# Kernel tuning notes

Measured on AMD Instinct MI355X. Metric: run time of the kernel, lower is better.

## Reference

```python
import jax, jax.numpy as jnp
import numpy as np

B, DIN, D, T, C = 32768, 784, 256, 16, 64


def setup_inputs() -> dict:
    key = jax.random.key(0)
    ks = jax.random.split(key, 4)
    x = jax.random.normal(ks[0], (B, DIN), dtype=jnp.float32)
    Wp = jax.random.normal(ks[1], (DIN, D), dtype=jnp.float32) / np.sqrt(DIN).astype(np.float32)
    bp = jnp.zeros((D,), jnp.float32)
    sigs_raw = jax.random.normal(ks[2], (T, D), dtype=jnp.float32) * 0.5
    Wc = jax.random.normal(ks[3], (T, D, C), dtype=jnp.float32) / np.sqrt(D).astype(np.float32)
    bc = jnp.zeros((T, C), jnp.float32)
    return {"x": x, "Wp": Wp, "bp": bp, "sigs_raw": sigs_raw, "Wc": Wc, "bc": bc}


def _quantize_ternary(s):
    # straight-through ternary quantization with +/-0.3 thresholds
    q = jnp.where(s > 0.3, 1.0, jnp.where(s < -0.3, -1.0, 0.0)).astype(s.dtype)
    return s + jax.lax.stop_gradient(q - s)


def reference(x, Wp, bp, sigs_raw, Wc, bc):
    h = x @ Wp + bp                                   # [B, D]
    sigs = _quantize_ternary(sigs_raw)                # [T, D] ternary signatures
    scores = h @ sigs.T                               # [B, T]
    tile_indices = jnp.argmax(scores, axis=-1)        # [B] top-1 routing
    # per-tile linear classifiers, then select the routed tile's logits
    all_logits = jnp.einsum('bd,tdc->btc', h, Wc) + bc[None]   # [B, T, C]
    logits = jnp.take_along_axis(all_logits, tile_indices[:, None, None], axis=1)[:, 0, :]
    return logits, tile_indices
```

## Files before the change

### kernel.cpp

```cpp
#include <hip/hip_runtime.h>

typedef short short8 __attribute__((ext_vector_type(8)));
typedef float f32x4 __attribute__((ext_vector_type(4)));

#define B_ROWS 32768
#define DIN 784
#define D_DIM 256
#define T_TILES 16
#define C_DIM 64
#define BM 64
#define NCHUNK 25

#define WPT_OFF    0u
#define WCT_OFF    409600u
#define WS_OFF     933888u
#define BS_OFF     1036288u
#define H_OFF      1036416u
#define BUCKET_OFF 17813632u
#define CNT_OFF    19910784u

static __device__ inline unsigned short f2bf(float f) {
    unsigned u = __builtin_bit_cast(unsigned, f);
    u += 0x7fffu + ((u >> 16) & 1u);
    return (unsigned short)(u >> 16);
}
static __device__ inline double qtern(float s) {
    double v = (double)s;
    return (v > 0.3) ? 1.0 : ((v < -0.3) ? -1.0 : 0.0);
}

__global__ __launch_bounds__(256)
void prep_kernel(const float* __restrict__ Wp, const float* __restrict__ bp,
                 const float* __restrict__ sigs_raw, const float* __restrict__ Wc,
                 char* __restrict__ ws) {
    __shared__ __align__(16) char u2[34816];
    const int bid = blockIdx.x, tid = threadIdx.x;
    unsigned short* wpt = (unsigned short*)(ws + WPT_OFF);
    unsigned short* wct = (unsigned short*)(ws + WCT_OFF);
    double* Wsd = (double*)(ws + WS_OFF);
    double* bsd = (double*)(ws + BS_OFF);

    if (bid < 25) {
        unsigned short (*lt)[40] = (unsigned short (*)[40])u2;
        const int k0 = bid * 32;
        #pragma unroll
        for (int p = 0; p < 8; ++p) {
            const int k = p * 4 + (tid >> 6);
            const int c = (tid & 63) * 4;
            float4 v = make_float4(0.f, 0.f, 0.f, 0.f);
            if (k0 + k < DIN) v = *(const float4*)&Wp[(size_t)(k0 + k) * D_DIM + c];
            lt[c + 0][k] = f2bf(v.x); lt[c + 1][k] = f2bf(v.y);
            lt[c + 2][k] = f2bf(v.z); lt[c + 3][k] = f2bf(v.w);
        }
        __syncthreads();
        const float4* src = (const float4*)&lt[tid][0];
        float4* dst = (float4*)(wpt + bid * 8192 + tid * 32);
        dst[0] = src[0]; dst[1] = src[1]; dst[2] = src[2]; dst[3] = src[3];
    } else if (bid < 123) {
        float* sigq = (float*)u2;
        float* wp8  = (float*)(u2 + 16384);
        const int k0 = (bid - 25) * 8;
        #pragma unroll
        for (int i = 0; i < 16; ++i) {
            const int idx = i * 256 + tid;
            sigq[idx] = (float)qtern(sigs_raw[idx]);
        }
        #pragma unroll
        for (int i = 0; i < 8; ++i)
            wp8[i * 256 + tid] = Wp[(size_t)(k0 + i) * D_DIM + tid];
        __syncthreads();
        const int kk = tid >> 5, t = (tid >> 1) & 15, half = tid & 1;
        double s = 0.0;
        const float* wr = &wp8[kk * 256 + half * 128];
        const float* sq = &sigq[t * 256 + half * 128];
        for (int d = 0; d < 128; ++d) s += (double)wr[d] * (double)sq[d];
        s += __shfl_xor(s, 1);
        if (half == 0) Wsd[(k0 + kk) * 16 + t] = s;
    } else if (bid < 139) {
        unsigned short (*lc)[264] = (unsigned short (*)[264])u2;
        const int t = bid - 123;
        #pragma unroll
        for (int j = 0; j < 16; ++j) {
            const int f4 = j * 256 + tid;
            const int d  = f4 >> 4;
            const int c4 = (f4 & 15) * 4;
            const float4 v = *(const float4*)&Wc[((size_t)t * D_DIM + d) * C_DIM + c4];
            lc[c4 + 0][d] = f2bf(v.x); lc[c4 + 1][d] = f2bf(v.y);
            lc[c4 + 2][d] = f2bf(v.z); lc[c4 + 3][d] = f2bf(v.w);
        }
        __syncthreads();
        const int c = tid >> 2, d0 = (tid & 3) * 64;
        const float4* src = (const float4*)&lc[c][d0];
        float4* dst = (float4*)(wct + t * 16384 + c * 256 + d0);
        #pragma unroll
        for (int i = 0; i < 8; ++i) dst[i] = src[i];
    } else {
        int* cnt = (int*)(ws + CNT_OFF);
        if (tid < 16) cnt[tid] = 0;
        Wsd[12544 + tid] = 0.0;
        const int t = tid >> 4, l = tid & 15;
        double s = 0.0;
        #pragma unroll
        for (int j = 0; j < 16; ++j) {
            const int d = l * 16 + j;
            s += (double)bp[d] * qtern(sigs_raw[t * D_DIM + d]);
        }
        #pragma unroll
        for (int m = 8; m >= 1; m >>= 1) s += __shfl_xor(s, m);
        if (l == 0) bsd[t] = s;
    }
}

__global__ __launch_bounds__(256, 2)
void gemm_score_kernel(const float* __restrict__ x, const float* __restrict__ bp,
                       char* __restrict__ ws, float* __restrict__ out) {
    __shared__ __align__(16) char u[59904];
    __shared__ int tidx_s[BM];

    unsigned short* Abuf = (unsigned short*)u;
    unsigned short* Bbuf = (unsigned short*)(u + 10240);
    double*         wss  = (double*)(u + 51200);

    const unsigned short* wpt = (const unsigned short*)(ws + WPT_OFF);
    unsigned short* hbf = (unsigned short*)(ws + H_OFF);
    const double* Wsd = (const double*)(ws + WS_OFF);
    const double* bsd = (const double*)(ws + BS_OFF);
    int* bucket = (int*)(ws + BUCKET_OFF);
    int* cnt = (int*)(ws + CNT_OFF);

    const int tid = threadIdx.x;
    const int row0 = blockIdx.x * BM;
    const int wid = tid >> 6, lane = tid & 63;
    const int wr = wid >> 1, wcid = wid & 1;
    const int lrow = lane & 15, kb8 = (lane >> 4) * 8;
    const int ar = tid >> 2, ako = (tid & 3) * 8;
    const int wk = tid >> 3, wt = (tid * 2) & 15;

    f32x4 acc[2][8];
    #pragma unroll
    for (int i = 0; i < 2; ++i)
        #pragma unroll
        for (int j = 0; j < 8; ++j) acc[i][j] = (f32x4){0.f, 0.f, 0.f, 0.f};
    double accd[16];
    #pragma unroll
    for (int t = 0; t < 16; ++t) accd[t] = 0.0;
    float xs8[8];

    {
        const float4* p = (const float4*)&x[(size_t)(row0 + ar) * DIN + ako];
        const float4 a0 = p[0], a1 = p[1];
        xs8[0] = a0.x; xs8[1] = a0.y; xs8[2] = a0.z; xs8[3] = a0.w;
        xs8[4] = a1.x; xs8[5] = a1.y; xs8[6] = a1.z; xs8[7] = a1.w;
        unsigned short tmp[8];
        #pragma unroll
        for (int i = 0; i < 8; ++i) tmp[i] = f2bf(xs8[i]);
        *(short8*)(Abuf + ar * 40 + ako) = *(short8*)tmp;
        const float4* q = (const float4*)(wpt + tid * 32);
        float4* db = (float4*)(Bbuf + tid * 40);
        db[0] = q[0]; db[1] = q[1]; db[2] = q[2]; db[3] = q[3];
        const double w0 = Wsd[tid * 2], w1 = Wsd[tid * 2 + 1];
        wss[wk * 17 + wt] = w0; wss[wk * 17 + wt + 1] = w1;
    }
    __syncthreads();

    for (int c = 0; c < NCHUNK; ++c) {
        const int cur = c & 1;
        const bool more = (c + 1 < NCHUNK);
        float4 va0, va1, vb0, vb1, vb2, vb3;
        double w0 = 0.0, w1 = 0.0;
        if (more) {
            const int kbase = (c + 1) * 32 + ako;
            if (kbase < DIN) {
                const float4* p = (const float4*)&x[(size_t)(row0 + ar) * DIN + kbase];
                va0 = p[0]; va1 = p[1];
            } else {
                va0 = make_float4(0, 0, 0, 0); va1 = make_float4(0, 0, 0, 0);
            }
            const float4* q = (const float4*)(wpt + (c + 1) * 8192 + tid * 32);
            vb0 = q[0]; vb1 = q[1]; vb2 = q[2]; vb3 = q[3];
            w0 = Wsd[(c + 1) * 512 + tid * 2];
            w1 = Wsd[(c + 1) * 512 + tid * 2 + 1];
        }
        {
            const unsigned short* Ab = Abuf + cur * 2560;
            const unsigned short* Bb = Bbuf + cur * 10240;
            const short8 af0 = *(const short8*)(Ab + (wr * 32 + lrow) * 40 + kb8);
            const short8 af1 = *(const short8*)(Ab + (wr * 32 + 16 + lrow) * 40 + kb8);
            #pragma unroll
            for (int cf = 0; cf < 8; ++cf) {
                const short8 bfr = *(const short8*)(Bb + (wcid * 128 + cf * 16 + lrow) * 40 + kb8);
                acc[0][cf] = __builtin_amdgcn_mfma_f32_16x16x32_bf16(af0, bfr, acc[0][cf], 0, 0, 0);
                acc[1][cf] = __builtin_amdgcn_mfma_f32_16x16x32_bf16(af1, bfr, acc[1][cf], 0, 0, 0);
            }
        }
        {
            const double* wbase = wss + cur * 544;
            #pragma unroll
            for (int i = 0; i < 8; ++i) {
                const double xv = (double)xs8[i];
                const double* wrow = wbase + (ako + i) * 17;
                #pragma unroll
                for (int t = 0; t < 16; ++t) accd[t] += xv * wrow[t];
            }
        }
        if (more) {
            xs8[0] = va0.x; xs8[1] = va0.y; xs8[2] = va0.z; xs8[3] = va0.w;
            xs8[4] = va1.x; xs8[5] = va1.y; xs8[6] = va1.z; xs8[7] = va1.w;
            unsigned short tmp[8];
            #pragma unroll
            for (int i = 0; i < 8; ++i) tmp[i] = f2bf(xs8[i]);
            *(short8*)(Abuf + (cur ^ 1) * 2560 + ar * 40 + ako) = *(short8*)tmp;
            float4* db = (float4*)(Bbuf + (cur ^ 1) * 10240 + tid * 40);
            db[0] = vb0; db[1] = vb1; db[2] = vb2; db[3] = vb3;
            wss[(cur ^ 1) * 544 + wk * 17 + wt] = w0;
            wss[(cur ^ 1) * 544 + wk * 17 + wt + 1] = w1;
        }
        __syncthreads();
    }

    unsigned short* h_s = (unsigned short*)u;
    #pragma unroll
    for (int cf = 0; cf < 8; ++cf) {
        const int gc = wcid * 128 + cf * 16 + lrow;
        const float bpv = bp[gc];
        #pragma unroll
        for (int rf = 0; rf < 2; ++rf) {
            const int lr = wr * 32 + rf * 16 + (lane >> 4) * 4;
            #pragma unroll
            for (int r = 0; r < 4; ++r)
                h_s[(lr + r) * 264 + gc] = f2bf(acc[rf][cf][r] + bpv);
        }
    }

    #pragma unroll
    for (int t = 0; t < 16; ++t) {
        accd[t] += __shfl_xor(accd[t], 1);
        accd[t] += __shfl_xor(accd[t], 2);
    }
    if ((tid & 3) == 0) {
        double best = -1.0e300; int bi = 0;
        #pragma unroll
        for (int t = 0; t < 16; ++t) {
            const double v = accd[t] + bsd[t];
            if (v > best) { best = v; bi = t; }
        }
        tidx_s[ar] = bi;
        out[(size_t)B_ROWS * C_DIM + row0 + ar] = (float)bi;
    }
    __syncthreads();

    {
        const int r = tid >> 2, q = tid & 3;
        const float4* src = (const float4*)(h_s + r * 264 + q * 64);
        float4 v[8];
        #pragma unroll
        for (int i = 0; i < 8; ++i) v[i] = src[i];
        float4* dst = (float4*)(hbf + (size_t)(row0 + r) * D_DIM + q * 64);
        #pragma unroll
        for (int i = 0; i < 8; ++i) dst[i] = v[i];
    }

    if (tid < T_TILES) {
        int c = 0;
        for (int r = 0; r < BM; ++r) c += (tidx_s[r] == tid);
        int pos = atomicAdd(&cnt[tid], c);
        for (int r = 0; r < BM; ++r)
            if (tidx_s[r] == tid) bucket[tid * B_ROWS + (pos++)] = row0 + r;
    }
}

__global__ __launch_bounds__(256)
void logits_kernel(const float* __restrict__ bc, const char* __restrict__ ws,
                   float* __restrict__ out) {
    __shared__ __align__(16) unsigned short As[128 * 136];
    __shared__ __align__(16) unsigned short Bs[64 * 136];
    __shared__ int rows_s[128];

    const int tid = threadIdx.x;
    const int t = blockIdx.x >> 8;
    const int c0 = (blockIdx.x & 255) * 128;
    const int* cnt = (const int*)(ws + CNT_OFF);
    const int cntv = cnt[t];
    if (c0 >= cntv) return;

    const int* bucket = (const int*)(ws + BUCKET_OFF);
    const unsigned short* hbf = (const unsigned short*)(ws + H_OFF);
    const unsigned short* wct = (const unsigned short*)(ws + WCT_OFF);

    if (tid < 128) {
        int i = c0 + tid; if (i >= cntv) i = cntv - 1;
        rows_s[tid] = bucket[t * B_ROWS + i];
    }
    __syncthreads();

    const int wid = tid >> 6, lane = tid & 63;
    const int wr = wid >> 1, wcid = wid & 1;
    const int lrow = lane & 15, kb8 = (lane >> 4) * 8;

    f32x4 acc[4][2];
    #pragma unroll
    for (int i = 0; i < 4; ++i) { acc[i][0] = (f32x4){0,0,0,0}; acc[i][1] = (f32x4){0,0,0,0}; }

    #pragma unroll
    for (int ch = 0; ch < 2; ++ch) {
        const int k0 = ch * 128;
        {
            const int r = tid >> 1, h64 = (tid & 1) * 64;
            const float4* p = (const float4*)(hbf + (size_t)rows_s[r] * D_DIM + k0 + h64);
            float4 v[8];
            #pragma unroll
            for (int i = 0; i < 8; ++i) v[i] = p[i];
            float4* d = (float4*)(As + r * 136 + h64);
            #pragma unroll
            for (int i = 0; i < 8; ++i) d[i] = v[i];
        }
        if (tid < 128) {
            const int c = tid >> 1, h64 = (tid & 1) * 64;
            const float4* p = (const float4*)(wct + (size_t)t * 16384 + c * 256 + k0 + h64);
            float4 v[8];
            #pragma unroll
            for (int i = 0; i < 8; ++i) v[i] = p[i];
            float4* d = (float4*)(Bs + c * 136 + h64);
            #pragma unroll
            for (int i = 0; i < 8; ++i) d[i] = v[i];
        }
        __syncthreads();
        #pragma unroll
        for (int ks = 0; ks < 4; ++ks) {
            const int kb = ks * 32 + kb8;
            const short8 bf0 = *(const short8*)(Bs + (wcid * 32 + lrow) * 136 + kb);
            const short8 bf1 = *(const short8*)(Bs + (wcid * 32 + 16 + lrow) * 136 + kb);
            #pragma unroll
            for (int rf = 0; rf < 4; ++rf) {
                const short8 af = *(const short8*)(As + (wr * 64 + rf * 16 + lrow) * 136 + kb);
                acc[rf][0] = __builtin_amdgcn_mfma_f32_16x16x32_bf16(af, bf0, acc[rf][0], 0, 0, 0);
                acc[rf][1] = __builtin_amdgcn_mfma_f32_16x16x32_bf16(af, bf1, acc[rf][1], 0, 0, 0);
            }
        }
        __syncthreads();
    }

    #pragma unroll
    for (int cf = 0; cf < 2; ++cf) {
        const int col = wcid * 32 + cf * 16 + lrow;
        const float bcv = bc[t * C_DIM + col];
        #pragma unroll
        for (int rf = 0; rf < 4; ++rf) {
            const int lr = wr * 64 + rf * 16 + (lane >> 4) * 4;
            #pragma unroll
            for (int r = 0; r < 4; ++r)
                out[(size_t)rows_s[lr + r] * C_DIM + col] = acc[rf][cf][r] + bcv;
        }
    }
}

extern "C" void kernel_launch(void* const* d_in, const int* in_sizes, int n_in,
                              void* d_out, int out_size, void* d_ws, size_t ws_size,
                              hipStream_t stream) {
    const float* x    = (const float*)d_in[0];
    const float* Wp   = (const float*)d_in[1];
    const float* bp   = (const float*)d_in[2];
    const float* sigs = (const float*)d_in[3];
    const float* Wc   = (const float*)d_in[4];
    const float* bc   = (const float*)d_in[5];
    float* out = (float*)d_out;
    char* ws = (char*)d_ws;

    prep_kernel<<<dim3(140), dim3(256), 0, stream>>>(Wp, bp, sigs, Wc, ws);
    gemm_score_kernel<<<dim3(B_ROWS / BM), dim3(256), 0, stream>>>(x, bp, ws, out);
    logits_kernel<<<dim3(16 * 256), dim3(256), 0, stream>>>(bc, ws, out);
}
```

Measured before the change: 235.8 us.

## Load Wp fragments straight from global, shrink LDS, retile logits kernel to 64 rows

The projection GEMM no longer stages the bf16 Wp chunk through shared memory. Each wave reads its MFMA B fragments directly from global/L2, which cuts LDS from about 59KB to 33KB and allows three blocks per CU. The fp64 score weights move to a padded double2 layout so each thread reads them as vector loads. The logits kernel now uses 64-row tiles with twice as many blocks and drops one barrier, trading more global traffic for Wc and Wp against higher occupancy and less padding waste in small buckets.

```diff
diff --git a/kernel.cpp b/kernel.cpp
--- a/kernel.cpp
+++ b/kernel.cpp
@@ -111,15 +111,14 @@
     }
 }
 
-__global__ __launch_bounds__(256, 2)
+__global__ __launch_bounds__(256, 3)
 void gemm_score_kernel(const float* __restrict__ x, const float* __restrict__ bp,
                        char* __restrict__ ws, float* __restrict__ out) {
-    __shared__ __align__(16) char u[59904];
+    __shared__ __align__(16) char u[33792];
     __shared__ int tidx_s[BM];
 
     unsigned short* Abuf = (unsigned short*)u;
-    unsigned short* Bbuf = (unsigned short*)(u + 10240);
-    double*         wss  = (double*)(u + 51200);
+    char* wssb = u + 10240;
 
     const unsigned short* wpt = (const unsigned short*)(ws + WPT_OFF);
     unsigned short* hbf = (unsigned short*)(ws + H_OFF);
@@ -133,8 +132,8 @@
     const int wid = tid >> 6, lane = tid & 63;
     const int wr = wid >> 1, wcid = wid & 1;
     const int lrow = lane & 15, kb8 = (lane >> 4) * 8;
-    const int ar = tid >> 2, ako = (tid & 3) * 8;
-    const int wk = tid >> 3, wt = (tid * 2) & 15;
+    const int ar = tid >> 2, aq = tid & 3, ako = aq * 8;
+    const int wtp = tid >> 5, wkk = tid & 31;
 
     f32x4 acc[2][8];
     #pragma unroll
@@ -145,6 +144,9 @@
     #pragma unroll
     for (int t = 0; t < 16; ++t) accd[t] = 0.0;
     float xs8[8];
+
+    const int wsoff = wtp * 576 + wkk * 16 + (wkk >> 3) * 16;
+    const char* wrd_base = wssb + aq * 144;
 
     {
         const float4* p = (const float4*)&x[(size_t)(row0 + ar) * DIN + ako];
@@ -155,19 +157,21 @@
         #pragma unroll
         for (int i = 0; i < 8; ++i) tmp[i] = f2bf(xs8[i]);
         *(short8*)(Abuf + ar * 40 + ako) = *(short8*)tmp;
-        const float4* q = (const float4*)(wpt + tid * 32);
-        float4* db = (float4*)(Bbuf + tid * 40);
-        db[0] = q[0]; db[1] = q[1]; db[2] = q[2]; db[3] = q[3];
-        const double w0 = Wsd[tid * 2], w1 = Wsd[tid * 2 + 1];
-        wss[wk * 17 + wt] = w0; wss[wk * 17 + wt + 1] = w1;
+        const double2 wv = *(const double2*)&Wsd[wkk * 16 + wtp * 2];
+        *(double2*)(wssb + wsoff) = wv;
     }
     __syncthreads();
 
     for (int c = 0; c < NCHUNK; ++c) {
         const int cur = c & 1;
         const bool more = (c + 1 < NCHUNK);
-        float4 va0, va1, vb0, vb1, vb2, vb3;
-        double w0 = 0.0, w1 = 0.0;
+
+        short8 bfr[8];
+        #pragma unroll
+        for (int cf = 0; cf < 8; ++cf)
+            bfr[cf] = *(const short8*)(wpt + c * 8192 + (wcid * 128 + cf * 16 + lrow) * 32 + kb8);
+
+        float4 va0, va1; double2 wv;
         if (more) {
             const int kbase = (c + 1) * 32 + ako;
             if (kbase < DIN) {
@@ -176,33 +180,34 @@
             } else {
                 va0 = make_float4(0, 0, 0, 0); va1 = make_float4(0, 0, 0, 0);
             }
-            const float4* q = (const float4*)(wpt + (c + 1) * 8192 + tid * 32);
-            vb0 = q[0]; vb1 = q[1]; vb2 = q[2]; vb3 = q[3];
-            w0 = Wsd[(c + 1) * 512 + tid * 2];
-            w1 = Wsd[(c + 1) * 512 + tid * 2 + 1];
-        }
+            wv = *(const double2*)&Wsd[((c + 1) * 32 + wkk) * 16 + wtp * 2];
+        }
+
+        {
+            const char* wb = wrd_base + cur * 4608;
+            #pragma unroll
+            for (int i = 0; i < 8; ++i) {
+                const double xd = (double)xs8[i];
+                #pragma unroll
+                for (int tp = 0; tp < 8; ++tp) {
+                    const double2 w2 = *(const double2*)(wb + tp * 576 + i * 16);
+                    accd[2 * tp]     += xd * w2.x;
+                    accd[2 * tp + 1] += xd * w2.y;
+                }
+            }
+        }
+
         {
             const unsigned short* Ab = Abuf + cur * 2560;
-            const unsigned short* Bb = Bbuf + cur * 10240;
             const short8 af0 = *(const short8*)(Ab + (wr * 32 + lrow) * 40 + kb8);
             const short8 af1 = *(const short8*)(Ab + (wr * 32 + 16 + lrow) * 40 + kb8);
             #pragma unroll
             for (int cf = 0; cf < 8; ++cf) {
-                const short8 bfr = *(const short8*)(Bb + (wcid * 128 + cf * 16 + lrow) * 40 + kb8);
-                acc[0][cf] = __builtin_amdgcn_mfma_f32_16x16x32_bf16(af0, bfr, acc[0][cf], 0, 0, 0);
-                acc[1][cf] = __builtin_amdgcn_mfma_f32_16x16x32_bf16(af1, bfr, acc[1][cf], 0, 0, 0);
+                acc[0][cf] = __builtin_amdgcn_mfma_f32_16x16x32_bf16(af0, bfr[cf], acc[0][cf], 0, 0, 0);
+                acc[1][cf] = __builtin_amdgcn_mfma_f32_16x16x32_bf16(af1, bfr[cf], acc[1][cf], 0, 0, 0);
             }
         }
-        {
-            const double* wbase = wss + cur * 544;
-            #pragma unroll
-            for (int i = 0; i < 8; ++i) {
-                const double xv = (double)xs8[i];
-                const double* wrow = wbase + (ako + i) * 17;
-                #pragma unroll
-                for (int t = 0; t < 16; ++t) accd[t] += xv * wrow[t];
-            }
-        }
+
         if (more) {
             xs8[0] = va0.x; xs8[1] = va0.y; xs8[2] = va0.z; xs8[3] = va0.w;
             xs8[4] = va1.x; xs8[5] = va1.y; xs8[6] = va1.z; xs8[7] = va1.w;
@@ -210,10 +215,7 @@
             #pragma unroll
             for (int i = 0; i < 8; ++i) tmp[i] = f2bf(xs8[i]);
             *(short8*)(Abuf + (cur ^ 1) * 2560 + ar * 40 + ako) = *(short8*)tmp;
-            float4* db = (float4*)(Bbuf + (cur ^ 1) * 10240 + tid * 40);
-            db[0] = vb0; db[1] = vb1; db[2] = vb2; db[3] = vb3;
-            wss[(cur ^ 1) * 544 + wk * 17 + wt] = w0;
-            wss[(cur ^ 1) * 544 + wk * 17 + wt + 1] = w1;
+            *(double2*)(wssb + (cur ^ 1) * 4608 + wsoff) = wv;
         }
         __syncthreads();
     }
@@ -237,7 +239,7 @@
         accd[t] += __shfl_xor(accd[t], 1);
         accd[t] += __shfl_xor(accd[t], 2);
     }
-    if ((tid & 3) == 0) {
+    if (aq == 0) {
         double best = -1.0e300; int bi = 0;
         #pragma unroll
         for (int t = 0; t < 16; ++t) {
@@ -269,16 +271,17 @@
     }
 }
 
+#define LBM 64
 __global__ __launch_bounds__(256)
 void logits_kernel(const float* __restrict__ bc, const char* __restrict__ ws,
                    float* __restrict__ out) {
-    __shared__ __align__(16) unsigned short As[128 * 136];
+    __shared__ __align__(16) unsigned short As[LBM * 136];
     __shared__ __align__(16) unsigned short Bs[64 * 136];
-    __shared__ int rows_s[128];
+    __shared__ int rows_s[LBM];
 
     const int tid = threadIdx.x;
-    const int t = blockIdx.x >> 8;
-    const int c0 = (blockIdx.x & 255) * 128;
+    const int t = blockIdx.x >> 9;
+    const int c0 = (blockIdx.x & 511) * LBM;
     const int* cnt = (const int*)(ws + CNT_OFF);
     const int cntv = cnt[t];
     if (c0 >= cntv) return;
@@ -287,7 +290,7 @@
     const unsigned short* hbf = (const unsigned short*)(ws + H_OFF);
     const unsigned short* wct = (const unsigned short*)(ws + WCT_OFF);
 
-    if (tid < 128) {
+    if (tid < LBM) {
         int i = c0 + tid; if (i >= cntv) i = cntv - 1;
         rows_s[tid] = bucket[t * B_ROWS + i];
     }
@@ -296,33 +299,33 @@
     const int wid = tid >> 6, lane = tid & 63;
     const int wr = wid >> 1, wcid = wid & 1;
     const int lrow = lane & 15, kb8 = (lane >> 4) * 8;
-
-    f32x4 acc[4][2];
-    #pragma unroll
-    for (int i = 0; i < 4; ++i) { acc[i][0] = (f32x4){0,0,0,0}; acc[i][1] = (f32x4){0,0,0,0}; }
+    const int sr = tid >> 2, sq = tid & 3;
+
+    f32x4 acc[2][2];
+    #pragma unroll
+    for (int i = 0; i < 2; ++i) { acc[i][0] = (f32x4){0,0,0,0}; acc[i][1] = (f32x4){0,0,0,0}; }
 
     #pragma unroll
     for (int ch = 0; ch < 2; ++ch) {
         const int k0 = ch * 128;
+        if (ch) __syncthreads();
         {
-            const int r = tid >> 1, h64 = (tid & 1) * 64;
-            const float4* p = (const float4*)(hbf + (size_t)rows_s[r] * D_DIM + k0 + h64);
-            float4 v[8];
-            #pragma unroll
-            for (int i = 0; i < 8; ++i) v[i] = p[i];
-            float4* d = (float4*)(As + r * 136 + h64);
-            #pragma unroll
-            for (int i = 0; i < 8; ++i) d[i] = v[i];
-        }
-        if (tid < 128) {
-            const int c = tid >> 1, h64 = (tid & 1) * 64;
-            const float4* p = (const float4*)(wct + (size_t)t * 16384 + c * 256 + k0 + h64);
-            float4 v[8];
-            #pragma unroll
-            for (int i = 0; i < 8; ++i) v[i] = p[i];
-            float4* d = (float4*)(Bs + c * 136 + h64);
-            #pragma unroll
-            for (int i = 0; i < 8; ++i) d[i] = v[i];
+            const float4* p = (const float4*)(hbf + (size_t)rows_s[sr] * D_DIM + k0 + sq * 32);
+            float4 v[4];
+            #pragma unroll
+            for (int i = 0; i < 4; ++i) v[i] = p[i];
+            float4* d = (float4*)(As + sr * 136 + sq * 32);
+            #pragma unroll
+            for (int i = 0; i < 4; ++i) d[i] = v[i];
+        }
+        {
+            const float4* p = (const float4*)(wct + (size_t)t * 16384 + sr * 256 + k0 + sq * 32);
+            float4 v[4];
+            #pragma unroll
+            for (int i = 0; i < 4; ++i) v[i] = p[i];
+            float4* d = (float4*)(Bs + sr * 136 + sq * 32);
+            #pragma unroll
+            for (int i = 0; i < 4; ++i) d[i] = v[i];
         }
         __syncthreads();
         #pragma unroll
@@ -331,13 +334,12 @@
             const short8 bf0 = *(const short8*)(Bs + (wcid * 32 + lrow) * 136 + kb);
             const short8 bf1 = *(const short8*)(Bs + (wcid * 32 + 16 + lrow) * 136 + kb);
             #pragma unroll
-            for (int rf = 0; rf < 4; ++rf) {
-                const short8 af = *(const short8*)(As + (wr * 64 + rf * 16 + lrow) * 136 + kb);
+            for (int rf = 0; rf < 2; ++rf) {
+                const short8 af = *(const short8*)(As + (wr * 32 + rf * 16 + lrow) * 136 + kb);
                 acc[rf][0] = __builtin_amdgcn_mfma_f32_16x16x32_bf16(af, bf0, acc[rf][0], 0, 0, 0);
                 acc[rf][1] = __builtin_amdgcn_mfma_f32_16x16x32_bf16(af, bf1, acc[rf][1], 0, 0, 0);
             }
         }
-        __syncthreads();
     }
 
     #pragma unroll
@@ -345,8 +347,8 @@
         const int col = wcid * 32 + cf * 16 + lrow;
         const float bcv = bc[t * C_DIM + col];
         #pragma unroll
-        for (int rf = 0; rf < 4; ++rf) {
-            const int lr = wr * 64 + rf * 16 + (lane >> 4) * 4;
+        for (int rf = 0; rf < 2; ++rf) {
+            const int lr = wr * 32 + rf * 16 + (lane >> 4) * 4;
             #pragma unroll
             for (int r = 0; r < 4; ++r)
                 out[(size_t)rows_s[lr + r] * C_DIM + col] = acc[rf][cf][r] + bcv;
@@ -368,5 +370,5 @@
 
     prep_kernel<<<dim3(140), dim3(256), 0, stream>>>(Wp, bp, sigs, Wc, ws);
     gemm_score_kernel<<<dim3(B_ROWS / BM), dim3(256), 0, stream>>>(x, bp, ws, out);
-    logits_kernel<<<dim3(16 * 256), dim3(256), 0, stream>>>(bc, ws, out);
-}
+    logits_kernel<<<dim3(16 * 512), dim3(256), 0, stream>>>(bc, ws, out);
+}
```

After: 239.1 us. About the same (+1.4%).
